# Optimization experiments

Hardware: AMD Instinct MI355X
Metric: run time of the kernel (lower is better)

Reference implementation:

```python
import jax, jax.numpy as jnp
import numpy as np

NUM_HEADS = 32
NUM_KV_HEADS = 8
HEAD_DIM = 128
SLIDING_WINDOW = 1024
ROPE_THETA = 10000.0


def _rotate_half(x):
    x1, x2 = jnp.split(x, 2, axis=-1)
    return jnp.concatenate((-x2, x1), axis=-1)


def _rope_cos_sin(seq_len, head_dim, theta, dtype):
    inv_freq = 1.0 / (theta ** (jnp.arange(0, head_dim, 2, dtype=jnp.float32) / head_dim))
    t = jnp.arange(seq_len, dtype=jnp.float32)
    freqs = t[:, None] * inv_freq[None, :]            # [S, hd/2]
    emb = jnp.concatenate((freqs, freqs), axis=-1)     # [S, hd]
    return jnp.cos(emb).astype(dtype), jnp.sin(emb).astype(dtype)


def setup_inputs() -> dict:
    key = jax.random.key(0)
    ks = jax.random.split(key, 5)
    B, S, H = 2, 2048, 4096
    kv_dim = NUM_KV_HEADS * HEAD_DIM
    scale = 1.0 / np.sqrt(H)
    return {
        "hidden_states": jax.random.normal(ks[0], (B, S, H), dtype=jnp.float32),
        "Wq": jax.random.normal(ks[1], (H, H), dtype=jnp.float32) * scale,
        "Wk": jax.random.normal(ks[2], (H, kv_dim), dtype=jnp.float32) * scale,
        "Wv": jax.random.normal(ks[3], (H, kv_dim), dtype=jnp.float32) * scale,
        "Wo": jax.random.normal(ks[4], (H, H), dtype=jnp.float32) * scale,
    }


def reference(hidden_states, Wq, Wk, Wv, Wo):
    B, S, H = hidden_states.shape
    groups = NUM_HEADS // NUM_KV_HEADS

    q = (hidden_states @ Wq).reshape(B, S, NUM_HEADS, HEAD_DIM).transpose(0, 2, 1, 3)
    k = (hidden_states @ Wk).reshape(B, S, NUM_KV_HEADS, HEAD_DIM).transpose(0, 2, 1, 3)
    v = (hidden_states @ Wv).reshape(B, S, NUM_KV_HEADS, HEAD_DIM).transpose(0, 2, 1, 3)

    cos, sin = _rope_cos_sin(S, HEAD_DIM, ROPE_THETA, q.dtype)  # [S, hd]
    q = q * cos + _rotate_half(q) * sin
    k = k * cos + _rotate_half(k) * sin

    # GQA: repeat_interleave kv heads to match query heads
    k = jnp.repeat(k, groups, axis=1)
    v = jnp.repeat(v, groups, axis=1)

    scores = jnp.einsum("bhqd,bhkd->bhqk", q, k) / np.sqrt(HEAD_DIM)

    i = jnp.arange(S)[:, None]
    j = jnp.arange(S)[None, :]
    allowed = (j <= i) & (i - j <= SLIDING_WINDOW // 2)  # causal + sliding window
    scores = jnp.where(allowed[None, None], scores, jnp.float32(-1e30))

    probs = jax.nn.softmax(scores, axis=-1)
    out = jnp.einsum("bhqk,bhkd->bhqd", probs, v)        # [B, nH, S, hd]
    out = out.transpose(0, 2, 1, 3).reshape(B, S, NUM_HEADS * HEAD_DIM)
    return out @ Wo
```

## Files before the change

### kernel.cpp

```cpp
#include <hip/hip_runtime.h>
#include <hip/hip_bf16.h>
#include <math.h>

#define BB 2
#define SS 2048
#define HH 4096
#define NH 32
#define NKV 8
#define HD 128
#define KVD (NKV*HD)
#define WIN 512
#define MROWS (BB*SS)

#define DT_BF16 1
#define DT_F32  2

typedef __hip_bfloat16 bf16;
typedef __attribute__((ext_vector_type(8))) short short8;
typedef __attribute__((ext_vector_type(4))) float f32x4;

__device__ __forceinline__ float ldf(const bf16* p){ return __bfloat162float(*p); }
__device__ __forceinline__ float ldf(const float* p){ return *p; }
__device__ __forceinline__ void stf(bf16* p, float v){ *p = __float2bfloat16(v); }
__device__ __forceinline__ void stf(float* p, float v){ *p = v; }

__global__ void detect_kernel(const void* __restrict__ w, int* __restrict__ flag)
{
  __shared__ int big;
  if (threadIdx.x == 0) big = 0;
  __syncthreads();
  const unsigned short* u = (const unsigned short*)w;
  for (int i = threadIdx.x; i < 2048; i += 256) {
    int ex = (u[i] >> 7) & 0xFF;
    if (ex >= 160) big = 1;
  }
  __syncthreads();
  if (threadIdx.x == 0) *flag = big ? DT_F32 : DT_BF16;
}

__global__ __launch_bounds__(256)
void cvt_x(const int* __restrict__ flag, const float* __restrict__ X,
           bf16* __restrict__ Y)
{
  if (*flag != DT_F32) return;
  const size_t idx = (size_t)blockIdx.x*256 + threadIdx.x;
  const f32x4 a = *(const f32x4*)(X + idx*8);
  const f32x4 b = *(const f32x4*)(X + idx*8 + 4);
  union { short8 s; bf16 h[8]; } u;
  #pragma unroll
  for (int j = 0; j < 4; j++) {
    u.h[j]     = __float2bfloat16(a[j]);
    u.h[j + 4] = __float2bfloat16(b[j]);
  }
  *(short8*)(Y + idx*8) = u.s;
}

__global__ __launch_bounds__(256)
void transpose_cvt(const int* __restrict__ flag,
                   const void* W0, const void* W1,
                   bf16* D0, bf16* D1, int Kd, int Nd)
{
  const bool isf32 = (*flag == DT_F32);
  const void* W = blockIdx.z ? W1 : W0;
  bf16*     WT  = blockIdx.z ? D1 : D0;
  __shared__ float tile[32][33];
  const int n0 = blockIdx.x*32, k0 = blockIdx.y*32;
  const int tx = threadIdx.x & 31, ty = threadIdx.x >> 5;
  #pragma unroll
  for (int j = 0; j < 4; j++) {
    const size_t off = (size_t)(k0 + ty + j*8)*Nd + n0 + tx;
    tile[ty + j*8][tx] = isf32 ? ((const float*)W)[off]
                               : __bfloat162float(((const bf16*)W)[off]);
  }
  __syncthreads();
  #pragma unroll
  for (int j = 0; j < 4; j++)
    WT[(size_t)(n0 + ty + j*8)*Kd + k0 + tx] = __float2bfloat16(tile[tx][ty + j*8]);
}

#define MFMA16(a,b,c) __builtin_amdgcn_mfma_f32_16x16x32_bf16(a,b,c,0,0,0)

template<int OUTF>
__global__ __launch_bounds__(512)
void gemm256(const int* __restrict__ flag,
             const bf16* __restrict__ Abf, const bf16* __restrict__ Axb,
             const bf16* __restrict__ Bm, void* __restrict__ C,
             int M, int N, int K)
{
  const bool isf32 = (*flag == DT_F32);
  const bf16* A = isf32 ? Axb : Abf;
  __shared__ __align__(16) bf16 lds[65536];
  const int tid = threadIdx.x;
  const int w = tid >> 6, lane = tid & 63;
  const int wm = w >> 2, wn = w & 3;
  const int fr = lane & 15, fq = lane >> 4;

  const int gx = gridDim.x;
  int wg = blockIdx.y*gx + blockIdx.x;
  const int cpx = (gx*gridDim.y) >> 3;
  wg = (wg & 7)*cpx + (wg >> 3);
  const int tM = (wg / gx)*256, tN = (wg % gx)*256;

  const int NT = K >> 6;

  auto stage = [&](int tt, int s){
    const int dbuf = tt & 1;
    const int hf = s & 1;
    const bf16* src = (s < 2) ? A : Bm;
    const int brow = ((s < 2) ? tM : tN) + hf*128;
    const int cbase = ((s < 2) ? 0 : 4096) + (dbuf*2 + hf)*1024;
    #pragma unroll
    for (int g = 0; g < 2; g++) {
      const int Ch = g*512 + tid;
      const int r = Ch >> 3, c = Ch & 7;
      const int cs = c ^ (r & 7);
      const bf16* gp = src + (size_t)(brow + r)*K + tt*64 + cs*8;
      char* lp = (char*)lds + (size_t)(cbase + g*512 + w*64)*16;
      __builtin_amdgcn_global_load_lds((const __attribute__((address_space(1))) void*)gp,
                                       (__attribute__((address_space(3))) void*)lp, 16, 0, 0);
    }
  };
  auto rdA = [&](int dbuf, int m, int kk) -> short8 {
    const int r = m*16 + fr;
    const int chunk = (dbuf*2 + wm)*1024 + r*8 + ((kk*4 + fq) ^ (r & 7));
    return *(const short8*)((char*)lds + (size_t)chunk*16);
  };
  auto rdB = [&](int dbuf, int n, int kk) -> short8 {
    const int rg = wn*64 + n*16 + fr;
    const int hf = rg >> 7, rr = rg & 127;
    const int chunk = 4096 + (dbuf*2 + hf)*1024 + rr*8 + ((kk*4 + fq) ^ (rr & 7));
    return *(const short8*)((char*)lds + (size_t)chunk*16);
  };

  f32x4 acc[8][4] = {};

  #pragma unroll
  for (int s = 0; s < 4; s++) stage(0, s);
  stage(1, 0); stage(1, 1);
  asm volatile("s_waitcnt vmcnt(4)" ::: "memory");
  __builtin_amdgcn_s_barrier();

  short8 a0[4][2], a1[4][2], b0[2][2], b1[2][2];
  for (int kt = 0; kt < NT; kt++) {
    const int db = kt & 1;
    #pragma unroll
    for (int m = 0; m < 4; m++){ a0[m][0]=rdA(db,m,0); a0[m][1]=rdA(db,m,1); }
    #pragma unroll
    for (int n = 0; n < 2; n++){ b0[n][0]=rdB(db,n,0); b0[n][1]=rdB(db,n,1); }
    if (kt+1 < NT) stage(kt+1, 2);
    asm volatile("s_waitcnt lgkmcnt(0)" ::: "memory");
    __builtin_amdgcn_sched_barrier(0);
    __builtin_amdgcn_s_setprio(1);
    #pragma unroll
    for (int m = 0; m < 4; m++)
      #pragma unroll
      for (int n = 0; n < 2; n++){
        acc[m][n] = MFMA16(a0[m][0], b0[n][0], acc[m][n]);
        acc[m][n] = MFMA16(a0[m][1], b0[n][1], acc[m][n]);
      }
    __builtin_amdgcn_s_setprio(0);
    __builtin_amdgcn_s_barrier();
    #pragma unroll
    for (int m = 0; m < 4; m++){ a1[m][0]=rdA(db,m+4,0); a1[m][1]=rdA(db,m+4,1); }
    #pragma unroll
    for (int n = 0; n < 2; n++){ b1[n][0]=rdB(db,n+2,0); b1[n][1]=rdB(db,n+2,1); }
    if (kt+1 < NT) stage(kt+1, 3);
    asm volatile("s_waitcnt lgkmcnt(0)" ::: "memory");
    __builtin_amdgcn_sched_barrier(0);
    __builtin_amdgcn_s_setprio(1);
    #pragma unroll
    for (int m = 0; m < 4; m++)
      #pragma unroll
      for (int n = 0; n < 2; n++){
        acc[m+4][n+2] = MFMA16(a1[m][0], b1[n][0], acc[m+4][n+2]);
        acc[m+4][n+2] = MFMA16(a1[m][1], b1[n][1], acc[m+4][n+2]);
      }
    __builtin_amdgcn_s_setprio(0);
    __builtin_amdgcn_s_barrier();
    if (kt+2 < NT) stage(kt+2, 0);
    __builtin_amdgcn_s_setprio(1);
    #pragma unroll
    for (int m = 0; m < 4; m++)
      #pragma unroll
      for (int n = 0; n < 2; n++){
        acc[m][n+2] = MFMA16(a0[m][0], b1[n][0], acc[m][n+2]);
        acc[m][n+2] = MFMA16(a0[m][1], b1[n][1], acc[m][n+2]);
      }
    __builtin_amdgcn_s_setprio(0);
    __builtin_amdgcn_s_barrier();
    if (kt+2 < NT) stage(kt+2, 1);
    __builtin_amdgcn_s_setprio(1);
    #pragma unroll
    for (int m = 0; m < 4; m++)
      #pragma unroll
      for (int n = 0; n < 2; n++){
        acc[m+4][n] = MFMA16(a1[m][0], b0[n][0], acc[m+4][n]);
        acc[m+4][n] = MFMA16(a1[m][1], b0[n][1], acc[m+4][n]);
      }
    __builtin_amdgcn_s_setprio(0);
    if (kt+2 < NT) { asm volatile("s_waitcnt vmcnt(4)" ::: "memory"); }
    else           { asm volatile("s_waitcnt vmcnt(0)" ::: "memory"); }
    __builtin_amdgcn_s_barrier();
  }

  #pragma unroll
  for (int m = 0; m < 8; m++)
    #pragma unroll
    for (int n = 0; n < 4; n++)
      #pragma unroll
      for (int r = 0; r < 4; r++) {
        const size_t off = (size_t)(tM + wm*128 + m*16 + fq*4 + r)*N
                         + (tN + wn*64 + n*16 + fr);
        if (OUTF && isf32) ((float*)C)[off] = acc[m][n][r];
        else               stf((bf16*)C + off, acc[m][n][r]);
      }
}

__global__ __launch_bounds__(256)
void gemm_kv(const int* __restrict__ flag,
             const bf16* __restrict__ Abf, const bf16* __restrict__ Axb,
             const bf16* __restrict__ WTk, const bf16* __restrict__ WTv,
             bf16* __restrict__ Kout, bf16* __restrict__ VTout, int M, int N, int K)
{
  const bf16* A = (*flag == DT_F32) ? Axb : Abf;
  const bool vpath = blockIdx.z != 0;
  const bf16* Bm = vpath ? WTv : WTk;
  __shared__ __align__(16) bf16 As[128*32];
  __shared__ __align__(16) bf16 Bs[128*32];
  const int tid  = threadIdx.x;
  const int w    = tid >> 6;
  const int lane = tid & 63;
  const int wr = w >> 1, wc = w & 1;
  const int tM = blockIdx.y*128, tN = blockIdx.x*128;
  const int srow = tid >> 2;
  const int scol = (tid & 3) * 8;
  const int fr = lane & 15;
  const int kq = (lane >> 4) * 8;

  f32x4 acc[4][4] = {};

  for (int k0 = 0; k0 < K; k0 += 32) {
    __syncthreads();
    #pragma unroll
    for (int q = 0; q < 2; q++) {
      const int row = q*64 + srow;
      const bf16* ga = A  + (size_t)(tM + row)*K + k0 + scol;
      const bf16* gb = Bm + (size_t)(tN + row)*K + k0 + scol;
      char* la = (char*)As + q*4096 + w*1024;
      char* lb = (char*)Bs + q*4096 + w*1024;
      __builtin_amdgcn_global_load_lds((const __attribute__((address_space(1))) void*)ga,
                                       (__attribute__((address_space(3))) void*)la, 16, 0, 0);
      __builtin_amdgcn_global_load_lds((const __attribute__((address_space(1))) void*)gb,
                                       (__attribute__((address_space(3))) void*)lb, 16, 0, 0);
    }
    __syncthreads();

    short8 af[4], bfr[4];
    #pragma unroll
    for (int m = 0; m < 4; m++) af[m]  = *(const short8*)&As[(wr*64 + m*16 + fr)*32 + kq];
    #pragma unroll
    for (int n = 0; n < 4; n++) bfr[n] = *(const short8*)&Bs[(wc*64 + n*16 + fr)*32 + kq];
    #pragma unroll
    for (int m = 0; m < 4; m++)
      #pragma unroll
      for (int n = 0; n < 4; n++)
        acc[m][n] = MFMA16(af[m], bfr[n], acc[m][n]);
  }

  const int fq = lane >> 4;
  #pragma unroll
  for (int m = 0; m < 4; m++)
    #pragma unroll
    for (int n = 0; n < 4; n++)
      #pragma unroll
      for (int r = 0; r < 4; r++) {
        const int gm = tM + wr*64 + m*16 + fq*4 + r;
        const int gn = tN + wc*64 + n*16 + fr;
        if (vpath) {
          size_t idx = ((size_t)((gm >> 11)*NKV + (gn >> 7)))*((size_t)HD*SS)
                     + (size_t)(gn & 127)*SS + (gm & 2047);
          stf(VTout + idx, acc[m][n][r]);
        } else {
          stf(Kout + (size_t)gm*N + gn, acc[m][n][r]);
        }
      }
}

__global__ void rope_kernel(bf16* __restrict__ Qb, bf16* __restrict__ Kb)
{
  int idx = blockIdx.x*blockDim.x + threadIdx.x;
  int total = MROWS * (NH + NKV) * 64;
  if (idx >= total) return;
  int f   = idx & 63;
  int rem = idx >> 6;
  int h   = rem % (NH + NKV);
  int row = rem / (NH + NKV);
  int s   = row & (SS - 1);
  float ang = (float)s * exp2f((float)f * -0.20762050593046014f);
  float sv, cv;
  __sincosf(ang, &sv, &cv);
  bf16* X; int nh2; int hh;
  if (h < NH) { X = Qb; hh = h; nh2 = NH; }
  else        { X = Kb; hh = h - NH; nh2 = NKV; }
  size_t base = (size_t)row*nh2*HD + (size_t)hh*HD;
  float x1 = ldf(X + base + f), x2 = ldf(X + base + 64 + f);
  stf(X + base + f,      x1*cv - x2*sv);
  stf(X + base + 64 + f, x2*cv + x1*sv);
}

__global__ __launch_bounds__(256, 3)
void attn_mfma(const bf16* __restrict__ Q, const bf16* __restrict__ K,
               const bf16* __restrict__ VT, bf16* __restrict__ Aout)
{
  int flat = (blockIdx.z*NH + blockIdx.y)*(SS/64) + blockIdx.x;
  flat = (flat & 7)*(BB*NH*(SS/64)/8) + (flat >> 3);
  const int i0 = (flat & 31) * 64;
  const int h  = (flat >> 5) & 31;
  const int b  = flat >> 10;
  const int kh = h >> 2;
  const int tid = threadIdx.x;
  const int w = tid >> 6, lane = tid & 63;
  const int fr = lane & 15, fq = lane >> 4;

  __shared__ __align__(16) bf16 Ks[64*128];
  __shared__ __align__(16) bf16 Vs[128*64];
  __shared__ __align__(16) bf16 Ps[4][16*64];

  const int qrow = w*16 + fr;
  const bf16* gq = Q + (size_t)(b*SS + i0 + qrow)*HH + h*HD + fq*8;
  short8 qf[4];
  #pragma unroll
  for (int kk = 0; kk < 4; kk++) qf[kk] = *(const short8*)(gq + kk*32);

  short8 kreg[4], vreg[4];
  auto loadKV = [&](int j0){
    const bf16* gk = K + (size_t)(b*SS + j0)*KVD + kh*HD;
    #pragma unroll
    for (int it = 0; it < 4; it++) {
      int slot = tid + it*256;
      int r = slot >> 4, cg = slot & 15;
      kreg[it] = *(const short8*)(gk + (size_t)r*KVD + cg*8);
    }
    const bf16* gv = VT + ((size_t)(b*NKV + kh)*HD)*SS + j0;
    #pragma unroll
    for (int it = 0; it < 4; it++) {
      int slot = tid + it*256;
      int d = slot >> 3, jg = slot & 7;
      vreg[it] = *(const short8*)(gv + (size_t)d*SS + jg*8);
    }
  };
  auto writeKV = [&](){
    #pragma unroll
    for (int it = 0; it < 4; it++) {
      int slot = tid + it*256;
      int r = slot >> 4, cg = slot & 15;
      *(short8*)((char*)Ks + r*256 + ((cg*16) ^ ((r & 7) << 4))) = kreg[it];
      int d = slot >> 3, jg = slot & 7;
      *(short8*)((char*)Vs + d*128 + ((jg*16) ^ ((d & 7) << 4))) = vreg[it];
    }
  };

  const float scale = 0.08838834764831845f;
  f32x4 o[8];
  #pragma unroll
  for (int nn = 0; nn < 8; nn++) o[nn] = (f32x4){0.f, 0.f, 0.f, 0.f};
  float m_run[4] = {-1e30f, -1e30f, -1e30f, -1e30f};
  float l_run[4] = {0.f, 0.f, 0.f, 0.f};

  const int j0_lo = (i0 >= WIN) ? (i0 - WIN) : 0;
  loadKV(j0_lo);

  for (int j0 = j0_lo; j0 <= i0; j0 += 64) {
    writeKV();
    __syncthreads();

    f32x4 sv[4];
    #pragma unroll
    for (int jf = 0; jf < 4; jf++) sv[jf] = (f32x4){0.f, 0.f, 0.f, 0.f};
    #pragma unroll
    for (int kk = 0; kk < 4; kk++) {
      #pragma unroll
      for (int jf = 0; jf < 4; jf++) {
        const int krow = jf*16 + fr;
        short8 kf = *(const short8*)((char*)Ks + krow*256 + ((kk*64 + fq*16) ^ ((krow & 7) << 4)));
        sv[jf] = MFMA16(qf[kk], kf, sv[jf]);
      }
    }

    if (j0 + 64 <= i0) loadKV(j0 + 64);

    const bool needmask = !((j0 >= i0 - 448) && (j0 <= i0 - 64));
    #pragma unroll
    for (int jf = 0; jf < 4; jf++)
      #pragma unroll
      for (int r = 0; r < 4; r++) {
        float x = sv[jf][r] * scale;
        if (needmask) {
          int iq = i0 + w*16 + fq*4 + r;
          int jv = j0 + jf*16 + fr;
          if (jv > iq || iq - jv > WIN) x = -1e30f;
        }
        sv[jf][r] = x;
      }

    float fac[4];
    #pragma unroll
    for (int r = 0; r < 4; r++) {
      float t = fmaxf(fmaxf(sv[0][r], sv[1][r]), fmaxf(sv[2][r], sv[3][r]));
      t = fmaxf(t, __shfl_xor(t, 1));
      t = fmaxf(t, __shfl_xor(t, 2));
      t = fmaxf(t, __shfl_xor(t, 4));
      t = fmaxf(t, __shfl_xor(t, 8));
      float mn = fmaxf(m_run[r], t);
      fac[r] = __expf(m_run[r] - mn);
      m_run[r] = mn;
    }
    #pragma unroll
    for (int r = 0; r < 4; r++) {
      float sum = 0.f;
      #pragma unroll
      for (int jf = 0; jf < 4; jf++) {
        float p = __expf(sv[jf][r] - m_run[r]);
        sv[jf][r] = p;
        sum += p;
      }
      sum += __shfl_xor(sum, 1);
      sum += __shfl_xor(sum, 2);
      sum += __shfl_xor(sum, 4);
      sum += __shfl_xor(sum, 8);
      l_run[r] = l_run[r]*fac[r] + sum;
    }

    char* pbase = (char*)(&Ps[w][0]);
    #pragma unroll
    for (int jf = 0; jf < 4; jf++)
      #pragma unroll
      for (int r = 0; r < 4; r++) {
        int q = fq*4 + r, j = jf*16 + fr;
        *(bf16*)(pbase + q*128 + ((j*2) ^ ((q & 7) << 4))) = __float2bfloat16(sv[jf][r]);
      }

    #pragma unroll
    for (int nn = 0; nn < 8; nn++)
      #pragma unroll
      for (int r = 0; r < 4; r++) o[nn][r] *= fac[r];

    #pragma unroll
    for (int kt = 0; kt < 2; kt++) {
      short8 ap = *(const short8*)(pbase + fr*128 + ((kt*64 + fq*16) ^ ((fr & 7) << 4)));
      #pragma unroll
      for (int nn = 0; nn < 8; nn++) {
        const int d = nn*16 + fr;
        short8 vf = *(const short8*)((char*)Vs + d*128 + ((kt*64 + fq*16) ^ ((d & 7) << 4)));
        o[nn] = MFMA16(ap, vf, o[nn]);
      }
    }
    __syncthreads();
  }

  float inv[4];
  #pragma unroll
  for (int r = 0; r < 4; r++) inv[r] = 1.0f / l_run[r];
  bf16* ao = Aout + (size_t)(b*SS + i0 + w*16)*HH + h*HD;
  #pragma unroll
  for (int nn = 0; nn < 8; nn++)
    #pragma unroll
    for (int r = 0; r < 4; r++)
      stf(ao + (size_t)(fq*4 + r)*HH + nn*16 + fr, o[nn][r] * inv[r]);
}

extern "C" void kernel_launch(void* const* d_in, const int* in_sizes, int n_in,
                              void* d_out, int out_size, void* d_ws, size_t ws_size,
                              hipStream_t stream)
{
  char* ws = (char*)d_ws;
  const size_t MB = (size_t)1 << 20;
  int*  flag = (int*)ws;
  bf16* Q  = (bf16*)(ws + 256);
  bf16* K  = (bf16*)(ws + 256 + 32*MB);
  bf16* VT = (bf16*)(ws + 256 + 40*MB);
  bf16* S  = (bf16*)(ws + 256 + 48*MB);
  bf16* WTk = S;
  bf16* WTv = S + (size_t)KVD*HH;
  bf16* WTo = Q;
  bf16* Xb = (bf16*)d_out;
  const bf16* X0 = (const bf16*)d_in[0];

  detect_kernel<<<1, 256, 0, stream>>>(d_in[1], flag);
  cvt_x<<<MROWS*HH/8/256, 256, 0, stream>>>(flag, (const float*)d_in[0], Xb);

  transpose_cvt<<<dim3(HH/32, HH/32, 1), 256, 0, stream>>>(flag, d_in[1], d_in[1], S, S, HH, HH);
  gemm256<0><<<dim3(HH/256, MROWS/256), 512, 0, stream>>>(flag, X0, Xb, S, Q, MROWS, HH, HH);

  transpose_cvt<<<dim3(KVD/32, HH/32, 2), 256, 0, stream>>>(flag, d_in[2], d_in[3], WTk, WTv, HH, KVD);
  gemm_kv<<<dim3(KVD/128, MROWS/128, 2), 256, 0, stream>>>(flag, X0, Xb, WTk, WTv, K, VT, MROWS, KVD, HH);

  rope_kernel<<<(MROWS*(NH+NKV)*64 + 255)/256, 256, 0, stream>>>(Q, K);
  attn_mfma<<<dim3(SS/64, NH, BB), 256, 0, stream>>>(Q, K, VT, S);

  transpose_cvt<<<dim3(HH/32, HH/32, 1), 256, 0, stream>>>(flag, d_in[4], d_in[4], WTo, WTo, HH, HH);
  gemm256<1><<<dim3(HH/256, MROWS/256), 512, 0, stream>>>(flag, S, S, WTo, d_out, MROWS, HH, HH);
}
```

Before: 736.4 us.

## Use 128-wide KV tiles and transposed QK MFMA in sliding-window attention

Doubles the key/value tile per loop iteration from 64 to 128, halving the number of barriers and loop iterations. The QK product operands are swapped so each lane holds scores for one query row, which turns the row max and sum reductions into two cross-lane shuffles and lets probabilities be packed into 4-wide LDS stores. The cost is more shared memory and registers (launch bounds lowered to 2 blocks per CU), clamped out-of-range loads, and more wasted masked work at the window edges.

```diff
diff --git a/kernel.cpp b/kernel.cpp
--- a/kernel.cpp
+++ b/kernel.cpp
@@ -18,6 +18,7 @@
 typedef __hip_bfloat16 bf16;
 typedef __attribute__((ext_vector_type(8))) short short8;
 typedef __attribute__((ext_vector_type(4))) float f32x4;
+typedef __attribute__((ext_vector_type(4))) unsigned short ushort4v;
 
 __device__ __forceinline__ float ldf(const bf16* p){ return __bfloat162float(*p); }
 __device__ __forceinline__ float ldf(const float* p){ return *p; }
@@ -308,7 +309,7 @@
   stf(X + base + 64 + f, x2*cv + x1*sv);
 }
 
-__global__ __launch_bounds__(256, 3)
+__global__ __launch_bounds__(256, 2)
 void attn_mfma(const bf16* __restrict__ Q, const bf16* __restrict__ K,
                const bf16* __restrict__ VT, bf16* __restrict__ Aout)
 {
@@ -322,9 +323,9 @@
   const int w = tid >> 6, lane = tid & 63;
   const int fr = lane & 15, fq = lane >> 4;
 
-  __shared__ __align__(16) bf16 Ks[64*128];
-  __shared__ __align__(16) bf16 Vs[128*64];
-  __shared__ __align__(16) bf16 Ps[4][16*64];
+  __shared__ __align__(16) bf16 Ks[128*128];
+  __shared__ __align__(16) bf16 Vs[128*128];
+  __shared__ __align__(16) bf16 Ps[4][16*128];
 
   const int qrow = w*16 + fr;
   const bf16* gq = Q + (size_t)(b*SS + i0 + qrow)*HH + h*HD + fq*8;
@@ -332,31 +333,25 @@
   #pragma unroll
   for (int kk = 0; kk < 4; kk++) qf[kk] = *(const short8*)(gq + kk*32);
 
-  short8 kreg[4], vreg[4];
+  short8 kreg[8], vreg[8];
   auto loadKV = [&](int j0){
-    const bf16* gk = K + (size_t)(b*SS + j0)*KVD + kh*HD;
-    #pragma unroll
-    for (int it = 0; it < 4; it++) {
+    #pragma unroll
+    for (int it = 0; it < 8; it++) {
       int slot = tid + it*256;
       int r = slot >> 4, cg = slot & 15;
-      kreg[it] = *(const short8*)(gk + (size_t)r*KVD + cg*8);
-    }
-    const bf16* gv = VT + ((size_t)(b*NKV + kh)*HD)*SS + j0;
-    #pragma unroll
-    for (int it = 0; it < 4; it++) {
-      int slot = tid + it*256;
-      int d = slot >> 3, jg = slot & 7;
-      vreg[it] = *(const short8*)(gv + (size_t)d*SS + jg*8);
+      int jr = j0 + r; jr = (jr < SS) ? jr : (SS - 1);
+      kreg[it] = *(const short8*)(K + (size_t)(b*SS + jr)*KVD + kh*HD + cg*8);
+      int s = j0 + cg*8; s = (s <= SS - 8) ? s : (SS - 8);
+      vreg[it] = *(const short8*)(VT + ((size_t)(b*NKV + kh)*HD + r)*SS + s);
     }
   };
   auto writeKV = [&](){
     #pragma unroll
-    for (int it = 0; it < 4; it++) {
+    for (int it = 0; it < 8; it++) {
       int slot = tid + it*256;
       int r = slot >> 4, cg = slot & 15;
       *(short8*)((char*)Ks + r*256 + ((cg*16) ^ ((r & 7) << 4))) = kreg[it];
-      int d = slot >> 3, jg = slot & 7;
-      *(short8*)((char*)Vs + d*128 + ((jg*16) ^ ((d & 7) << 4))) = vreg[it];
+      *(short8*)((char*)Vs + r*256 + ((cg*16) ^ ((r & 7) << 4))) = vreg[it];
     }
   };
 
@@ -364,103 +359,107 @@
   f32x4 o[8];
   #pragma unroll
   for (int nn = 0; nn < 8; nn++) o[nn] = (f32x4){0.f, 0.f, 0.f, 0.f};
-  float m_run[4] = {-1e30f, -1e30f, -1e30f, -1e30f};
-  float l_run[4] = {0.f, 0.f, 0.f, 0.f};
+  float m_run = -1e30f;
+  float l_run = 0.f;
 
   const int j0_lo = (i0 >= WIN) ? (i0 - WIN) : 0;
   loadKV(j0_lo);
 
-  for (int j0 = j0_lo; j0 <= i0; j0 += 64) {
+  const int iq = i0 + w*16 + fr;
+
+  for (int j0 = j0_lo; j0 <= i0; j0 += 128) {
     writeKV();
     __syncthreads();
 
-    f32x4 sv[4];
-    #pragma unroll
-    for (int jf = 0; jf < 4; jf++) sv[jf] = (f32x4){0.f, 0.f, 0.f, 0.f};
+    f32x4 sv[8];
+    #pragma unroll
+    for (int jf = 0; jf < 8; jf++) sv[jf] = (f32x4){0.f, 0.f, 0.f, 0.f};
     #pragma unroll
     for (int kk = 0; kk < 4; kk++) {
       #pragma unroll
-      for (int jf = 0; jf < 4; jf++) {
+      for (int jf = 0; jf < 8; jf++) {
         const int krow = jf*16 + fr;
         short8 kf = *(const short8*)((char*)Ks + krow*256 + ((kk*64 + fq*16) ^ ((krow & 7) << 4)));
-        sv[jf] = MFMA16(qf[kk], kf, sv[jf]);
-      }
-    }
-
-    if (j0 + 64 <= i0) loadKV(j0 + 64);
-
-    const bool needmask = !((j0 >= i0 - 448) && (j0 <= i0 - 64));
-    #pragma unroll
-    for (int jf = 0; jf < 4; jf++)
+        sv[jf] = MFMA16(kf, qf[kk], sv[jf]);
+      }
+    }
+
+    if (j0 + 128 <= i0) loadKV(j0 + 128);
+
+    const bool needmask = !((j0 >= i0 - 448) && (j0 <= i0 - 128));
+    #pragma unroll
+    for (int jf = 0; jf < 8; jf++)
       #pragma unroll
       for (int r = 0; r < 4; r++) {
         float x = sv[jf][r] * scale;
         if (needmask) {
-          int iq = i0 + w*16 + fq*4 + r;
-          int jv = j0 + jf*16 + fr;
+          int jv = j0 + jf*16 + fq*4 + r;
           if (jv > iq || iq - jv > WIN) x = -1e30f;
         }
         sv[jf][r] = x;
       }
 
-    float fac[4];
-    #pragma unroll
-    for (int r = 0; r < 4; r++) {
-      float t = fmaxf(fmaxf(sv[0][r], sv[1][r]), fmaxf(sv[2][r], sv[3][r]));
-      t = fmaxf(t, __shfl_xor(t, 1));
-      t = fmaxf(t, __shfl_xor(t, 2));
-      t = fmaxf(t, __shfl_xor(t, 4));
-      t = fmaxf(t, __shfl_xor(t, 8));
-      float mn = fmaxf(m_run[r], t);
-      fac[r] = __expf(m_run[r] - mn);
-      m_run[r] = mn;
-    }
-    #pragma unroll
-    for (int r = 0; r < 4; r++) {
-      float sum = 0.f;
-      #pragma unroll
-      for (int jf = 0; jf < 4; jf++) {
-        float p = __expf(sv[jf][r] - m_run[r]);
+    float t = -1e30f;
+    #pragma unroll
+    for (int jf = 0; jf < 8; jf++)
+      #pragma unroll
+      for (int r = 0; r < 4; r++) t = fmaxf(t, sv[jf][r]);
+    t = fmaxf(t, __shfl_xor(t, 16));
+    t = fmaxf(t, __shfl_xor(t, 32));
+    const float mn = fmaxf(m_run, t);
+    const float fac = __expf(m_run - mn);
+    m_run = mn;
+    float sum = 0.f;
+    #pragma unroll
+    for (int jf = 0; jf < 8; jf++)
+      #pragma unroll
+      for (int r = 0; r < 4; r++) {
+        float p = __expf(sv[jf][r] - mn);
         sv[jf][r] = p;
         sum += p;
       }
-      sum += __shfl_xor(sum, 1);
-      sum += __shfl_xor(sum, 2);
-      sum += __shfl_xor(sum, 4);
-      sum += __shfl_xor(sum, 8);
-      l_run[r] = l_run[r]*fac[r] + sum;
-    }
+    sum += __shfl_xor(sum, 16);
+    sum += __shfl_xor(sum, 32);
+    l_run = l_run*fac + sum;
 
     char* pbase = (char*)(&Ps[w][0]);
     #pragma unroll
-    for (int jf = 0; jf < 4; jf++)
+    for (int jf = 0; jf < 8; jf++) {
+      ushort4v pk;
       #pragma unroll
       for (int r = 0; r < 4; r++) {
-        int q = fq*4 + r, j = jf*16 + fr;
-        *(bf16*)(pbase + q*128 + ((j*2) ^ ((q & 7) << 4))) = __float2bfloat16(sv[jf][r]);
-      }
-
+        union { bf16 bx; unsigned short sx; } cv;
+        cv.bx = __float2bfloat16(sv[jf][r]);
+        pk[r] = cv.sx;
+      }
+      *(ushort4v*)(pbase + fr*256 + ((jf*32 + fq*8) ^ ((fr & 7) << 4))) = pk;
+    }
+
+    float fr4[4];
+    #pragma unroll
+    for (int r = 0; r < 4; r++) fr4[r] = __shfl(fac, fq*4 + r);
     #pragma unroll
     for (int nn = 0; nn < 8; nn++)
       #pragma unroll
-      for (int r = 0; r < 4; r++) o[nn][r] *= fac[r];
-
-    #pragma unroll
-    for (int kt = 0; kt < 2; kt++) {
-      short8 ap = *(const short8*)(pbase + fr*128 + ((kt*64 + fq*16) ^ ((fr & 7) << 4)));
+      for (int r = 0; r < 4; r++) o[nn][r] *= fr4[r];
+
+    #pragma unroll
+    for (int kt = 0; kt < 4; kt++) {
+      short8 ap = *(const short8*)(pbase + fr*256 + ((kt*64 + fq*16) ^ ((fr & 7) << 4)));
       #pragma unroll
       for (int nn = 0; nn < 8; nn++) {
         const int d = nn*16 + fr;
-        short8 vf = *(const short8*)((char*)Vs + d*128 + ((kt*64 + fq*16) ^ ((d & 7) << 4)));
+        short8 vf = *(const short8*)((char*)Vs + d*256 + ((kt*64 + fq*16) ^ ((d & 7) << 4)));
         o[nn] = MFMA16(ap, vf, o[nn]);
       }
     }
     __syncthreads();
   }
 
+  const float linv = 1.0f / l_run;
   float inv[4];
   #pragma unroll
-  for (int r = 0; r < 4; r++) inv[r] = 1.0f / l_run[r];
+  for (int r = 0; r < 4; r++) inv[r] = __shfl(linv, fq*4 + r);
   bf16* ao = Aout + (size_t)(b*SS + i0 + w*16)*HH + h*HD;
   #pragma unroll
   for (int nn = 0; nn < 8; nn++)
```

Result: faster. 696.0 us (-5.5%).
